# Kernel tuning notes

Measured on AMD Instinct MI355X. Metric: run time of the kernel, lower is better.

The kernel has to match this reference:

```python
import jax, jax.numpy as jnp
import numpy as np

B, T, C = 4, 2048, 1024
H = 16
D = C // H  # head_size = 64


def setup_inputs() -> dict:
    key = jax.random.key(0)
    ks = jax.random.split(key, 6)
    s = 0.02
    x = jax.random.normal(ks[0], (B, T, C), dtype=jnp.float32)
    # per-head projections (bias=False), stacked over heads: [H, C, D]
    Wq = jax.random.normal(ks[1], (H, C, D), dtype=jnp.float32) * s
    Wk = jax.random.normal(ks[2], (H, C, D), dtype=jnp.float32) * s
    Wv = jax.random.normal(ks[3], (H, C, D), dtype=jnp.float32) * s
    # output projection Linear(H*D, C)
    Wo = jax.random.normal(ks[4], (H * D, C), dtype=jnp.float32) * s
    bo = jax.random.normal(ks[5], (C,), dtype=jnp.float32) * s
    return {"x": x, "Wq": Wq, "Wk": Wk, "Wv": Wv, "Wo": Wo, "bo": bo}


def reference(x, Wq, Wk, Wv, Wo, bo):
    # q,k,v: [B, H, T, D]
    q = jnp.einsum('btc,hcd->bhtd', x, Wq)
    k = jnp.einsum('btc,hcd->bhtd', x, Wk)
    v = jnp.einsum('btc,hcd->bhtd', x, Wv)
    scale = 1.0 / jnp.sqrt(jnp.asarray(D, dtype=x.dtype))
    scores = jnp.einsum('bhtd,bhsd->bhts', q, k) * scale  # [B,H,T,T]
    causal = jnp.tril(jnp.ones((T, T), dtype=bool))
    scores = jnp.where(causal, scores, jnp.asarray(-jnp.inf, dtype=scores.dtype))
    wei = jax.nn.softmax(scores, axis=-1)
    out = jnp.einsum('bhts,bhsd->bhtd', wei, v)  # [B,H,T,D]
    # concat heads along last dim (head order = module list order)
    out = jnp.transpose(out, (0, 2, 1, 3)).reshape(B, T, H * D)
    return out @ Wo + bo
```

## Files before the change

kernel.cpp:

```cpp
#include <hip/hip_runtime.h>
#include <math.h>

typedef __attribute__((ext_vector_type(8))) short short8;
typedef __attribute__((ext_vector_type(4))) short short4v;
typedef __attribute__((ext_vector_type(4))) float floatx4;

#define AS1 __attribute__((address_space(1)))
#define AS3 __attribute__((address_space(3)))

__device__ inline void gload_lds16(const short* g, short* l) {
    __builtin_amdgcn_global_load_lds((const AS1 unsigned int*)g,
                                     (AS3 unsigned int*)l, 16, 0, 0);
}

__device__ inline short f2bf(float f) {
    unsigned u = __builtin_bit_cast(unsigned, f);
    u += 0x7fffu + ((u >> 16) & 1u);
    return (short)(u >> 16);
}

__global__ __launch_bounds__(256) void conv_x(
    const float* __restrict__ x, short* __restrict__ xb)
{
    int i = (blockIdx.x * 256 + threadIdx.x) * 4;
    float4 v = *(const float4*)&x[i];
    short4v o = { f2bf(v.x), f2bf(v.y), f2bf(v.z), f2bf(v.w) };
    *(short4v*)&xb[i] = o;
}

__global__ __launch_bounds__(256) void transpose_w(
    const float* __restrict__ Wq, const float* __restrict__ Wk,
    const float* __restrict__ Wv, const float* __restrict__ Wo,
    short* __restrict__ Wall, short* __restrict__ WoT)
{
    __shared__ short T[64 * 72];
    const int kt = blockIdx.x, y = blockIdx.y;
    const int tid = threadIdx.x;
    const int lr = tid >> 2, lc = (tid & 3) * 16;
    #pragma unroll 1
    for (int m = 0; m < 4; ++m) {
        const float* src;
        float s = 1.f;
        if (m < 3) {
            const float* W = (m == 0) ? Wq : (m == 1) ? Wk : Wv;
            src = W + ((size_t)y << 16) + (size_t)(kt * 64 + lr) * 64 + lc;
            if (m == 0) s = 0.125f * 1.44269504088896f;
        } else {
            src = Wo + (size_t)(kt * 64 + lr) * 1024 + y * 64 + lc;
        }
        short8 t0, t1;
        {
            float4 v0 = *(const float4*)(src + 0);
            float4 v1 = *(const float4*)(src + 4);
            float4 v2 = *(const float4*)(src + 8);
            float4 v3 = *(const float4*)(src + 12);
            t0[0]=f2bf(v0.x*s); t0[1]=f2bf(v0.y*s); t0[2]=f2bf(v0.z*s); t0[3]=f2bf(v0.w*s);
            t0[4]=f2bf(v1.x*s); t0[5]=f2bf(v1.y*s); t0[6]=f2bf(v1.z*s); t0[7]=f2bf(v1.w*s);
            t1[0]=f2bf(v2.x*s); t1[1]=f2bf(v2.y*s); t1[2]=f2bf(v2.z*s); t1[3]=f2bf(v2.w*s);
            t1[4]=f2bf(v3.x*s); t1[5]=f2bf(v3.y*s); t1[6]=f2bf(v3.z*s); t1[7]=f2bf(v3.w*s);
        }
        *(short8*)&T[lr * 72 + lc]     = t0;
        *(short8*)&T[lr * 72 + lc + 8] = t1;
        __syncthreads();
        short8 o0, o1;
        #pragma unroll
        for (int j = 0; j < 8; ++j) o0[j] = T[(lc + j) * 72 + lr];
        #pragma unroll
        for (int j = 0; j < 8; ++j) o1[j] = T[(lc + 8 + j) * 72 + lr];
        short* dst = (m < 3)
            ? Wall + (size_t)(m * 1024 + y * 64 + lr) * 1024 + kt * 64
            : WoT  + (size_t)(y * 64 + lr) * 1024 + kt * 64;
        *(short8*)&dst[lc]     = o0;
        *(short8*)&dst[lc + 8] = o1;
        __syncthreads();
    }
}

__global__ __launch_bounds__(256) void gemm_bt(
    const short* __restrict__ A, const short* __restrict__ BT,
    short* __restrict__ C, short* __restrict__ Vt, int M, int N, int K)
{
    __shared__ short As[128 * 64];
    __shared__ short Bs[128 * 64];
    const int tid  = threadIdx.x;
    const int wid  = tid >> 6, lane = tid & 63;
    const int quad = lane >> 4, l15 = lane & 15;
    const int l7 = l15 & 7;
    const int m0 = blockIdx.x * 128, n0 = blockIdx.y * 128;
    const int wr = (wid >> 1) * 64, wc = (wid & 1) * 64;

    floatx4 acc[4][4] = {};

    const int srow = tid >> 3;
    const int gcol = ((tid & 7) ^ (srow & 7)) * 8;

    for (int k0 = 0; k0 < K; k0 += 64) {
        #pragma unroll
        for (int t = 0; t < 4; ++t) {
            gload_lds16(A  + (size_t)(m0 + srow + t * 32) * K + k0 + gcol,
                        &As[(t * 32 + wid * 8) * 64]);
            gload_lds16(BT + (size_t)(n0 + srow + t * 32) * K + k0 + gcol,
                        &Bs[(t * 32 + wid * 8) * 64]);
        }
        __syncthreads();
        #pragma unroll
        for (int ks = 0; ks < 2; ++ks) {
            short8 bfr[4];
            #pragma unroll
            for (int j = 0; j < 4; ++j)
                bfr[j] = *(const short8*)&Bs[(wc + j * 16 + l15) * 64 +
                                             (((ks * 4 + quad) ^ l7) * 8)];
            #pragma unroll
            for (int i = 0; i < 4; ++i) {
                short8 afr = *(const short8*)&As[(wr + i * 16 + l15) * 64 +
                                                 (((ks * 4 + quad) ^ l7) * 8)];
                #pragma unroll
                for (int j = 0; j < 4; ++j)
                    acc[i][j] = __builtin_amdgcn_mfma_f32_16x16x32_bf16(
                        afr, bfr[j], acc[i][j], 0, 0, 0);
            }
        }
        __syncthreads();
    }

    const int plane = n0 >> 10;
    #pragma unroll
    for (int i = 0; i < 4; ++i) {
        int row = m0 + wr + i * 16 + quad * 4;
        #pragma unroll
        for (int j = 0; j < 4; ++j) {
            int col = n0 + wc + j * 16 + l15;
            int c1 = col & 1023;
            if (plane < 2) {
                short* dst = C + (size_t)plane * 8192 * 1024;
                #pragma unroll
                for (int r = 0; r < 4; ++r)
                    dst[(size_t)(row + r) * 1024 + c1] = f2bf(acc[i][j][r]);
            } else {
                int b = row >> 11, t = row & 2047;
                int hb = b * 16 + (c1 >> 6), d = c1 & 63;
                short4v o = { f2bf(acc[i][j][0]), f2bf(acc[i][j][1]),
                              f2bf(acc[i][j][2]), f2bf(acc[i][j][3]) };
                *(short4v*)&Vt[((size_t)hb * 64 + d) * 2048 + t] = o;
            }
        }
    }
}

__global__ __launch_bounds__(256) void gemm_o(
    const short* __restrict__ A, const short* __restrict__ BT,
    float* __restrict__ Cf, const float* __restrict__ bias, int N, int K)
{
    __shared__ short As[64 * 64];
    __shared__ short Bs[128 * 64];
    const int tid  = threadIdx.x;
    const int wid  = tid >> 6, lane = tid & 63;
    const int quad = lane >> 4, l15 = lane & 15;
    const int l7 = l15 & 7;
    const int flat = blockIdx.x;
    const int xcd = flat & 7, local = flat >> 3;
    const int m0 = local * 64, n0 = xcd * 128;
    const int wr = (wid >> 1) * 32, wc = (wid & 1) * 64;

    floatx4 acc[2][4] = {};

    const int srow = tid >> 3;
    const int gcol = ((tid & 7) ^ (srow & 7)) * 8;

    for (int k0 = 0; k0 < K; k0 += 64) {
        #pragma unroll
        for (int t = 0; t < 2; ++t)
            gload_lds16(A + (size_t)(m0 + srow + t * 32) * K + k0 + gcol,
                        &As[(t * 32 + wid * 8) * 64]);
        #pragma unroll
        for (int t = 0; t < 4; ++t)
            gload_lds16(BT + (size_t)(n0 + srow + t * 32) * K + k0 + gcol,
                        &Bs[(t * 32 + wid * 8) * 64]);
        __syncthreads();
        #pragma unroll
        for (int ks = 0; ks < 2; ++ks) {
            short8 bfr[4];
            #pragma unroll
            for (int j = 0; j < 4; ++j)
                bfr[j] = *(const short8*)&Bs[(wc + j * 16 + l15) * 64 +
                                             (((ks * 4 + quad) ^ l7) * 8)];
            #pragma unroll
            for (int i = 0; i < 2; ++i) {
                short8 afr = *(const short8*)&As[(wr + i * 16 + l15) * 64 +
                                                 (((ks * 4 + quad) ^ l7) * 8)];
                #pragma unroll
                for (int j = 0; j < 4; ++j)
                    acc[i][j] = __builtin_amdgcn_mfma_f32_16x16x32_bf16(
                        afr, bfr[j], acc[i][j], 0, 0, 0);
            }
        }
        __syncthreads();
    }

    #pragma unroll
    for (int i = 0; i < 2; ++i) {
        int row = m0 + wr + i * 16 + quad * 4;
        #pragma unroll
        for (int j = 0; j < 4; ++j) {
            int col = n0 + wc + j * 16 + l15;
            float bv = bias[col];
            #pragma unroll
            for (int r = 0; r < 4; ++r)
                Cf[(size_t)(row + r) * N + col] = acc[i][j][r] + bv;
        }
    }
}

__global__ __launch_bounds__(256) void attn_fwd(
    const short* __restrict__ Q, const short* __restrict__ Kg,
    const short* __restrict__ Vt_g, short* __restrict__ O)
{
    __shared__ short Ks[2][64 * 64];
    __shared__ short Vs[2][64 * 64];
    __shared__ short Pb[4 * 32 * 72];
    const int tid  = threadIdx.x;
    const int wid  = tid >> 6, lane = tid & 63;
    const int quad = lane >> 4, l15 = lane & 15;

    const int flat = blockIdx.x;
    const int xr = flat & 7;
    const int qq = flat >> 3;
    const int qt = 15 - (qq >> 3);
    const int hb = xr * 8 + (qq & 7);
    const int h = hb & 15, b = hb >> 4;

    const size_t base  = ((size_t)b * 2048) * 1024 + h * 64;
    const size_t vbase = ((size_t)(b * 16 + h)) * 64 * 2048;
    short* Pw = &Pb[wid * 32 * 72];

    const int srow = tid >> 3;
    const int gcol = ((tid & 7) ^ (srow & 7)) * 8;
    const int lbase0 = (wid * 8) * 64;
    const int lbase1 = (wid * 8 + 32) * 64;
    const int l7 = l15 & 7;

    const short one_bf = (short)0x3F80;
    const short8 bones = { one_bf, one_bf, one_bf, one_bf,
                           one_bf, one_bf, one_bf, one_bf };

    short8 qf[2][2];
    #pragma unroll
    for (int mt = 0; mt < 2; ++mt)
        #pragma unroll
        for (int ks = 0; ks < 2; ++ks)
            qf[mt][ks] = *(const short8*)&Q[base +
                (size_t)(qt * 128 + wid * 32 + mt * 16 + l15) * 1024 + ks * 32 + quad * 8];

    floatx4 oacc[2][4] = {};
    floatx4 lacc[2] = {};
    const int dst = 2 * qt + (wid >> 1);
    const int nst = 2 * qt + 2;

    const short* kptr = Kg + base + (size_t)srow * 1024 + gcol;
    const short* vptr = Vt_g + vbase + (size_t)srow * 2048 + gcol;

    gload_lds16(kptr,               &Ks[0][lbase0]);
    gload_lds16(kptr + 32 * 1024,   &Ks[0][lbase1]);
    gload_lds16(vptr,               &Vs[0][lbase0]);
    gload_lds16(vptr + 32 * 2048,   &Vs[0][lbase1]);
    kptr += 64 * 1024; vptr += 64;
    __syncthreads();

    for (int st = 0; st < nst; ++st) {
        const short* K0 = Ks[st & 1];
        const short* V0 = Vs[st & 1];
        if (st + 1 < nst) {
            short* K1 = Ks[(st + 1) & 1];
            short* V1 = Vs[(st + 1) & 1];
            gload_lds16(kptr,             &K1[lbase0]);
            gload_lds16(kptr + 32 * 1024, &K1[lbase1]);
            gload_lds16(vptr,             &V1[lbase0]);
            gload_lds16(vptr + 32 * 2048, &V1[lbase1]);
            kptr += 64 * 1024; vptr += 64;
        }

        if (st <= dst) {
            floatx4 sf[2][4];
            #pragma unroll
            for (int nt = 0; nt < 4; ++nt) {
                floatx4 z0 = {}, z1 = {};
                #pragma unroll
                for (int ks = 0; ks < 2; ++ks) {
                    short8 kfr = *(const short8*)&K0[(nt * 16 + l15) * 64 +
                                                     (((ks * 4 + quad) ^ l7) * 8)];
                    z0 = __builtin_amdgcn_mfma_f32_16x16x32_bf16(kfr, qf[0][ks], z0, 0, 0, 0);
                    z1 = __builtin_amdgcn_mfma_f32_16x16x32_bf16(kfr, qf[1][ks], z1, 0, 0, 0);
                }
                sf[0][nt] = z0; sf[1][nt] = z1;
            }

            if (st == dst) {
                #pragma unroll
                for (int mt = 0; mt < 2; ++mt)
                    #pragma unroll
                    for (int nt = 0; nt < 4; ++nt)
                        #pragma unroll
                        for (int r = 0; r < 4; ++r) {
                            int qa = qt * 128 + wid * 32 + mt * 16 + l15;
                            int sa = st * 64 + nt * 16 + quad * 4 + r;
                            if (sa > qa) sf[mt][nt][r] = -INFINITY;
                        }
            }

            #pragma unroll
            for (int mt = 0; mt < 2; ++mt)
                #pragma unroll
                for (int nt = 0; nt < 4; ++nt) {
                    unsigned p0 = __builtin_bit_cast(unsigned, __builtin_amdgcn_exp2f(sf[mt][nt][0]));
                    unsigned p1 = __builtin_bit_cast(unsigned, __builtin_amdgcn_exp2f(sf[mt][nt][1]));
                    unsigned p2 = __builtin_bit_cast(unsigned, __builtin_amdgcn_exp2f(sf[mt][nt][2]));
                    unsigned p3 = __builtin_bit_cast(unsigned, __builtin_amdgcn_exp2f(sf[mt][nt][3]));
                    uint2 w;
                    w.x = __builtin_amdgcn_perm(p1, p0, 0x07060302u);
                    w.y = __builtin_amdgcn_perm(p3, p2, 0x07060302u);
                    *(uint2*)&Pw[(mt * 16 + l15) * 72 +
                                 ((nt ^ (l15 >> 2)) * 16) + quad * 4] = w;
                }

            #pragma unroll
            for (int ks = 0; ks < 2; ++ks) {
                int blk = (ks * 2 + (quad >> 1)) ^ (l15 >> 2);
                short8 af0 = *(const short8*)&Pw[(l15) * 72 + blk * 16 + (quad & 1) * 8];
                short8 af1 = *(const short8*)&Pw[(16 + l15) * 72 + blk * 16 + (quad & 1) * 8];
                lacc[0] = __builtin_amdgcn_mfma_f32_16x16x32_bf16(af0, bones, lacc[0], 0, 0, 0);
                lacc[1] = __builtin_amdgcn_mfma_f32_16x16x32_bf16(af1, bones, lacc[1], 0, 0, 0);
                #pragma unroll
                for (int nt = 0; nt < 4; ++nt) {
                    short8 bfr = *(const short8*)&V0[(nt * 16 + l15) * 64 +
                                                     (((ks * 4 + quad) ^ l7) * 8)];
                    oacc[0][nt] = __builtin_amdgcn_mfma_f32_16x16x32_bf16(af0, bfr, oacc[0][nt], 0, 0, 0);
                    oacc[1][nt] = __builtin_amdgcn_mfma_f32_16x16x32_bf16(af1, bfr, oacc[1][nt], 0, 0, 0);
                }
            }
        }
        __syncthreads();
    }

    #pragma unroll
    for (int mt = 0; mt < 2; ++mt)
        #pragma unroll
        for (int nt = 0; nt < 4; ++nt)
            #pragma unroll
            for (int r = 0; r < 4; ++r) {
                float v = oacc[mt][nt][r] / lacc[mt][r];
                int qa = qt * 128 + wid * 32 + mt * 16 + quad * 4 + r;
                O[base + (size_t)qa * 1024 + nt * 16 + l15] = f2bf(v);
            }
}

extern "C" void kernel_launch(void* const* d_in, const int* in_sizes, int n_in,
                              void* d_out, int out_size, void* d_ws, size_t ws_size,
                              hipStream_t stream) {
    const float* x  = (const float*)d_in[0];
    const float* Wq = (const float*)d_in[1];
    const float* Wk = (const float*)d_in[2];
    const float* Wv = (const float*)d_in[3];
    const float* Wo = (const float*)d_in[4];
    const float* bo = (const float*)d_in[5];
    float* out = (float*)d_out;

    char* ws = (char*)d_ws;
    const size_t MB = 1024 * 1024;
    short* xb   = (short*)(ws + 0 * MB);
    short* Ao   = (short*)(ws + 0 * MB);
    short* Vt_g = (short*)(ws + 16 * MB);
    short* Wall = (short*)(ws + 32 * MB);
    short* WoT  = (short*)(ws + 38 * MB);
    short* Qp   = (short*)d_out;
    short* Kp   = Qp + 8 * 1024 * 1024;

    conv_x<<<8192, 256, 0, stream>>>(x, xb);
    transpose_w<<<dim3(16, 16), 256, 0, stream>>>(Wq, Wk, Wv, Wo, Wall, WoT);

    gemm_bt<<<dim3(64, 24), 256, 0, stream>>>(xb, Wall, Qp, Vt_g, 8192, 3072, 1024);

    attn_fwd<<<1024, 256, 0, stream>>>(Qp, Kp, Vt_g, Ao);

    gemm_o<<<1024, 256, 0, stream>>>(Ao, WoT, out, bo, 1024, 1024);
}
```

Baseline: 249.3 us.

## Double-buffer LDS in projection GEMM with K-step of 32

Rewrites the bf16 GEMM main loop to use two LDS buffers of 128x32 tiles. The next tile is prefetched with global_load_lds while MFMAs run on the current one, and one barrier per iteration replaces two. The goal is to hide global memory latency behind compute. The cost is a smaller K tile, which doubles the iteration count, plus a different swizzle. There is also a possible race: the async LDS loads may need a wait that the single __syncthreads does not guarantee.

```diff
diff --git a/kernel.cpp b/kernel.cpp
--- a/kernel.cpp
+++ b/kernel.cpp
@@ -80,48 +80,58 @@
     const short* __restrict__ A, const short* __restrict__ BT,
     short* __restrict__ C, short* __restrict__ Vt, int M, int N, int K)
 {
-    __shared__ short As[128 * 64];
-    __shared__ short Bs[128 * 64];
+    __shared__ short As[2][128 * 32];
+    __shared__ short Bs[2][128 * 32];
     const int tid  = threadIdx.x;
     const int wid  = tid >> 6, lane = tid & 63;
     const int quad = lane >> 4, l15 = lane & 15;
-    const int l7 = l15 & 7;
     const int m0 = blockIdx.x * 128, n0 = blockIdx.y * 128;
     const int wr = (wid >> 1) * 64, wc = (wid & 1) * 64;
 
     floatx4 acc[4][4] = {};
 
-    const int srow = tid >> 3;
-    const int gcol = ((tid & 7) ^ (srow & 7)) * 8;
-
-    for (int k0 = 0; k0 < K; k0 += 64) {
-        #pragma unroll
-        for (int t = 0; t < 4; ++t) {
-            gload_lds16(A  + (size_t)(m0 + srow + t * 32) * K + k0 + gcol,
-                        &As[(t * 32 + wid * 8) * 64]);
-            gload_lds16(BT + (size_t)(n0 + srow + t * 32) * K + k0 + gcol,
-                        &Bs[(t * 32 + wid * 8) * 64]);
-        }
-        __syncthreads();
-        #pragma unroll
-        for (int ks = 0; ks < 2; ++ks) {
-            short8 bfr[4];
+    const int srow = tid >> 2;
+    const int gcol = ((tid & 3) ^ (srow & 3)) * 8;
+    const int lrow0 = (wid * 16) * 32;
+    const int lrow1 = (wid * 16 + 64) * 32;
+    const int l3 = l15 & 3;
+    const int NT = K >> 5;
+
+    const short* aCur = A  + (size_t)(m0 + srow) * K + gcol;
+    const short* bCur = BT + (size_t)(n0 + srow) * K + gcol;
+
+#define STAGE(c) do { \
+    gload_lds16(aCur,                   &As[c][lrow0]); \
+    gload_lds16(aCur + (size_t)64 * K,  &As[c][lrow1]); \
+    gload_lds16(bCur,                   &Bs[c][lrow0]); \
+    gload_lds16(bCur + (size_t)64 * K,  &Bs[c][lrow1]); \
+    aCur += 32; bCur += 32; } while (0)
+
+    STAGE(0);
+    __syncthreads();
+
+    for (int t = 0; t < NT; ++t) {
+        if (t + 1 < NT) STAGE((t + 1) & 1);
+        const short* Ab = As[t & 1];
+        const short* Bb = Bs[t & 1];
+        short8 bfr[4], afr[4];
+        #pragma unroll
+        for (int j = 0; j < 4; ++j)
+            bfr[j] = *(const short8*)&Bb[(wc + j * 16 + l15) * 32 +
+                                         ((quad ^ l3) * 8)];
+        #pragma unroll
+        for (int i = 0; i < 4; ++i)
+            afr[i] = *(const short8*)&Ab[(wr + i * 16 + l15) * 32 +
+                                         ((quad ^ l3) * 8)];
+        #pragma unroll
+        for (int i = 0; i < 4; ++i)
             #pragma unroll
             for (int j = 0; j < 4; ++j)
-                bfr[j] = *(const short8*)&Bs[(wc + j * 16 + l15) * 64 +
-                                             (((ks * 4 + quad) ^ l7) * 8)];
-            #pragma unroll
-            for (int i = 0; i < 4; ++i) {
-                short8 afr = *(const short8*)&As[(wr + i * 16 + l15) * 64 +
-                                                 (((ks * 4 + quad) ^ l7) * 8)];
-                #pragma unroll
-                for (int j = 0; j < 4; ++j)
-                    acc[i][j] = __builtin_amdgcn_mfma_f32_16x16x32_bf16(
-                        afr, bfr[j], acc[i][j], 0, 0, 0);
-            }
-        }
-        __syncthreads();
-    }
+                acc[i][j] = __builtin_amdgcn_mfma_f32_16x16x32_bf16(
+                    afr[i], bfr[j], acc[i][j], 0, 0, 0);
+        __syncthreads();
+    }
+#undef STAGE
 
     const int plane = n0 >> 10;
     #pragma unroll
```

Result: no change. 253.6 us (+1.7%).
